# Optimization experiments

Measured on AMD Instinct MI355X. Metric: run time of the kernel, lower is better.

The kernel has to match this reference:

```python
import jax, jax.numpy as jnp
import numpy as np

N = 50000
E = 800000
IN_C = 128
HID = 128
HID2 = 256
OUT_C = 40


def setup_inputs() -> dict:
    key = jax.random.key(0)
    ks = jax.random.split(key, 12)
    x = jax.random.normal(ks[0], (N, IN_C), dtype=jnp.float32)
    edge_index = jax.random.randint(ks[1], (2, E), 0, N, dtype=jnp.int64)
    def lin(k, fi, fo):
        # torch Linear default init: U(-1/sqrt(fi), 1/sqrt(fi))
        b = 1.0 / np.sqrt(fi)
        k1, k2 = jax.random.split(k)
        W = jax.random.uniform(k1, (fi, fo), minval=-b, maxval=b, dtype=jnp.float32)
        bvec = jax.random.uniform(k2, (fo,), minval=-b, maxval=b, dtype=jnp.float32)
        return W, bvec
    W1, b1 = lin(ks[2], IN_C, HID)
    W2, b2 = lin(ks[3], HID, HID)
    W3, b3 = lin(ks[4], HID, HID2)
    W4, b4 = lin(ks[5], HID2, HID2)
    Wl, bl = lin(ks[6], HID2, OUT_C)
    return {"x": x, "edge_index": edge_index,
            "W1": W1, "b1": b1, "W2": W2, "b2": b2,
            "W3": W3, "b3": b3, "W4": W4, "b4": b4,
            "Wl": Wl, "bl": bl}


def gin_conv(x, src, dst, Wa, ba, Wb, bb):
    # GINConv, eps=0: h_i = MLP(x_i + sum_{j->i} x_j)
    agg = jax.ops.segment_sum(x[src], dst, num_segments=N)  # [N, d]
    h = x + agg
    h = jax.nn.relu(h @ Wa + ba)
    return h @ Wb + bb


def reference(x, edge_index, W1, b1, W2, b2, W3, b3, W4, b4, Wl, bl):
    src, dst = edge_index[0], edge_index[1]
    h = jax.nn.relu(gin_conv(x, src, dst, W1, b1, W2, b2))
    # dropout p=0.5 is identity in eval mode
    h = jax.nn.relu(gin_conv(h, src, dst, W3, b3, W4, b4))
    return h @ Wl + bl
```

## Files before the change

### kernel.cpp

```cpp
#include <hip/hip_runtime.h>
#include <hip/hip_bf16.h>
#include <hip/hip_fp16.h>
#include <stdint.h>

#define N_NODES 50000
#define E_EDGES 800000
#define NBKT 196
#define PBUF 6144

typedef short s16x8 __attribute__((ext_vector_type(8)));
typedef _Float16 f16x8 __attribute__((ext_vector_type(8)));
typedef float f32x4 __attribute__((ext_vector_type(4)));

__device__ __forceinline__ unsigned short f2h_bits(float f) {
    return __half_as_ushort(__float2half(f));
}
__device__ __forceinline__ float h2f(unsigned short u) {
    __half h = *reinterpret_cast<const __half*>(&u);
    return __half2float(h);
}
__device__ __forceinline__ float2 h2f2(unsigned int u) {
    __half2 h = *reinterpret_cast<const __half2*>(&u);
    return __half22float2(h);
}

__global__ __launch_bounds__(256) void khist_conv(
    const int* __restrict__ dst, int* __restrict__ gbcnt,
    const float* __restrict__ x, unsigned short* __restrict__ xh) {
    __shared__ int bcnt[NBKT];
    int t = threadIdx.x;
    for (int i = t; i < NBKT; i += 256) bcnt[i] = 0;
    __syncthreads();
    int gid = blockIdx.x * 256 + t;
    const int STRIDE = 256 * 256;
    const float4* xv = (const float4*)x;
    for (int e = gid; e < E_EDGES; e += STRIDE) {
        atomicAdd(&bcnt[dst[e] >> 8], 1);
        float4 a = xv[(size_t)2 * e];
        float4 b = xv[(size_t)2 * e + 1];
        s16x8 h;
        h[0] = (short)f2h_bits(a.x); h[1] = (short)f2h_bits(a.y);
        h[2] = (short)f2h_bits(a.z); h[3] = (short)f2h_bits(a.w);
        h[4] = (short)f2h_bits(b.x); h[5] = (short)f2h_bits(b.y);
        h[6] = (short)f2h_bits(b.z); h[7] = (short)f2h_bits(b.w);
        *(s16x8*)(xh + (size_t)e * 8) = h;
    }
    __syncthreads();
    for (int i = t; i < NBKT; i += 256) atomicAdd(&gbcnt[i], bcnt[i]);
}

__global__ void scan_bkt(const int* __restrict__ gbcnt, int* __restrict__ bscan,
                         int* __restrict__ gcur) {
    __shared__ int wsum[4];
    int t = threadIdx.x, lane = t & 63, wid = t >> 6;
    int v = (t < NBKT) ? gbcnt[t] : 0;
    int x = v;
#pragma unroll
    for (int off = 1; off < 64; off <<= 1) {
        int tt = __shfl_up(x, off);
        if (lane >= off) x += tt;
    }
    if (lane == 63) wsum[wid] = x;
    __syncthreads();
    if (t == 0) {
        int s = 0;
#pragma unroll
        for (int i = 0; i < 4; i++) { int tmp = wsum[i]; wsum[i] = s; s += tmp; }
    }
    __syncthreads();
    int excl = x - v + wsum[wid];
    if (t <= NBKT) bscan[t] = excl;
    if (t < NBKT) gcur[t] = excl;
}

__global__ __launch_bounds__(256) void bin_pass(
    const int* __restrict__ src, const int* __restrict__ dst,
    int* __restrict__ gcur, unsigned int* __restrict__ pool) {
    __shared__ unsigned int lbuf[NBKT][64];
    __shared__ int lcnt[NBKT];
    __shared__ int lbase[NBKT];
    int tid = threadIdx.x;
    for (int i = tid; i < NBKT; i += 256) lcnt[i] = 0;
    __syncthreads();
    const int EPG = (E_EDGES + gridDim.x - 1) / gridDim.x;
    int e0 = blockIdx.x * EPG;
    int e1 = e0 + EPG; if (e1 > E_EDGES) e1 = E_EDGES;
    for (int wbase = e0; wbase < e1; wbase += 2048) {
        int wend = wbase + 2048; if (wend > e1) wend = e1;
        int d8[8], s8[8], n8 = 0;
        {
            int e = wbase + tid;
#pragma unroll
            for (int k = 0; k < 8; k++, e += 256)
                if (e < wend) { d8[n8] = dst[e]; s8[n8] = src[e]; n8++; }
        }
        for (int k = 0; k < n8; k++) {
            int d = d8[k];
            unsigned int rec = (unsigned int)(s8[k] & 0xFFFF) |
                               ((unsigned int)(d & 255) << 16);
            int b = d >> 8;
            int slot = atomicAdd(&lcnt[b], 1);
            if (slot < 64) lbuf[b][slot] = rec;
            else pool[atomicAdd(&gcur[b], 1)] = rec;
        }
        __syncthreads();
        if (tid < NBKT) {
            int c = lcnt[tid]; if (c > 64) c = 64;
            int lines = c >> 5;
            if (lines) lbase[tid] = atomicAdd(&gcur[tid], lines * 32);
        }
        __syncthreads();
        {
            int wid = tid >> 6, lane = tid & 63;
            for (int b = wid * 49; b < (wid + 1) * 49; b++) {
                int c = lcnt[b]; if (c > 64) c = 64;
                int lines = c >> 5, rem = c & 31;
                for (int l = 0; l < lines; l++)
                    if (lane < 32)
                        pool[lbase[b] + l * 32 + lane] = lbuf[b][l * 32 + lane];
                if (lines && lane < rem) lbuf[b][lane] = lbuf[b][lines * 32 + lane];
                if (lane == 0) lcnt[b] = rem;
            }
        }
        __syncthreads();
    }
    if (tid < NBKT) {
        int c = lcnt[tid]; if (c > 64) c = 64;
        if (c) lbase[tid] = atomicAdd(&gcur[tid], c);
    }
    __syncthreads();
    {
        int wid = tid >> 6, lane = tid & 63;
        for (int b = wid * 49; b < (wid + 1) * 49; b++) {
            int c = lcnt[b]; if (c > 64) c = 64;
            if (lane < c) pool[lbase[b] + lane] = lbuf[b][lane];
        }
    }
}

__global__ __launch_bounds__(256) void build_csr(
    const unsigned int* __restrict__ pool, const int* __restrict__ bscan,
    int* __restrict__ rowptr, unsigned short* __restrict__ perm) {
    __shared__ int ncnt[256];
    __shared__ int ncur[256];
    __shared__ int wsum[4];
    __shared__ unsigned short pbuf[PBUF];
    int b = blockIdx.x, t = threadIdx.x;
    int base = bscan[b], K = bscan[b + 1] - base;
    ncnt[t] = 0;
    __syncthreads();
    for (int i = t; i < K; i += 256)
        atomicAdd(&ncnt[(pool[base + i] >> 16) & 255], 1);
    __syncthreads();
    int lane = t & 63, wid = t >> 6;
    int v = ncnt[t], x = v;
#pragma unroll
    for (int off = 1; off < 64; off <<= 1) {
        int tt = __shfl_up(x, off);
        if (lane >= off) x += tt;
    }
    if (lane == 63) wsum[wid] = x;
    __syncthreads();
    if (t == 0) {
        int s = 0;
#pragma unroll
        for (int i = 0; i < 4; i++) { int tmp = wsum[i]; wsum[i] = s; s += tmp; }
    }
    __syncthreads();
    int excl = x - v + wsum[wid];
    int node = b * 256 + t;
    if (node <= N_NODES) rowptr[node] = base + excl;
    ncur[t] = excl;
    __syncthreads();
    for (int i = t; i < K; i += 256) {
        unsigned int rec = pool[base + i];
        int nl = (rec >> 16) & 255;
        int pos = atomicAdd(&ncur[nl], 1);
        if (pos < PBUF) pbuf[pos] = (unsigned short)rec;
        else perm[base + pos] = (unsigned short)rec;
    }
    __syncthreads();
    int KK = K < PBUF ? K : PBUF;
    for (int i = t; i < KK; i += 256) perm[base + i] = pbuf[i];
}

__global__ __launch_bounds__(256) void gather_agg_h(
    const unsigned short* __restrict__ feat,
    const int* __restrict__ rowptr,
    const unsigned short* __restrict__ perm,
    unsigned short* __restrict__ out) {
    int node = (blockIdx.x * 256 + threadIdx.x) >> 6;
    if (node >= N_NODES) return;
    int lane = threadIdx.x & 63;
    const unsigned int* fv = (const unsigned int*)feat;
    float2 acc = h2f2(fv[(size_t)node * 64 + lane]);
    int beg = rowptr[node], end = rowptr[node + 1];
    for (int base = beg; base < end; base += 64) {
        int cnt = end - base; if (cnt > 64) cnt = 64;
        int pv = (base + lane < end) ? (int)perm[base + lane] : 0;
        int j = 0;
        for (; j + 7 < cnt; j += 8) {
            int s0 = __shfl(pv, j);
            int s1 = __shfl(pv, j + 1);
            int s2 = __shfl(pv, j + 2);
            int s3 = __shfl(pv, j + 3);
            int s4 = __shfl(pv, j + 4);
            int s5 = __shfl(pv, j + 5);
            int s6 = __shfl(pv, j + 6);
            int s7 = __shfl(pv, j + 7);
            unsigned int u0 = fv[(size_t)s0 * 64 + lane];
            unsigned int u1 = fv[(size_t)s1 * 64 + lane];
            unsigned int u2 = fv[(size_t)s2 * 64 + lane];
            unsigned int u3 = fv[(size_t)s3 * 64 + lane];
            unsigned int u4 = fv[(size_t)s4 * 64 + lane];
            unsigned int u5 = fv[(size_t)s5 * 64 + lane];
            unsigned int u6 = fv[(size_t)s6 * 64 + lane];
            unsigned int u7 = fv[(size_t)s7 * 64 + lane];
            float2 f0 = h2f2(u0), f1 = h2f2(u1), f2 = h2f2(u2), f3 = h2f2(u3);
            float2 f4 = h2f2(u4), f5 = h2f2(u5), f6 = h2f2(u6), f7 = h2f2(u7);
            acc.x += (f0.x + f1.x) + (f2.x + f3.x);
            acc.y += (f0.y + f1.y) + (f2.y + f3.y);
            acc.x += (f4.x + f5.x) + (f6.x + f7.x);
            acc.y += (f4.y + f5.y) + (f6.y + f7.y);
        }
        for (; j + 1 < cnt; j += 2) {
            int s0 = __shfl(pv, j);
            int s1 = __shfl(pv, j + 1);
            unsigned int u0 = fv[(size_t)s0 * 64 + lane];
            unsigned int u1 = fv[(size_t)s1 * 64 + lane];
            float2 f0 = h2f2(u0), f1 = h2f2(u1);
            acc.x += f0.x + f1.x;
            acc.y += f0.y + f1.y;
        }
        if (j < cnt) {
            int s = __shfl(pv, j);
            float2 f = h2f2(fv[(size_t)s * 64 + lane]);
            acc.x += f.x;
            acc.y += f.y;
        }
    }
    unsigned int o = (unsigned int)f2h_bits(acc.x) | ((unsigned int)f2h_bits(acc.y) << 16);
    ((unsigned int*)out)[(size_t)node * 64 + lane] = o;
}

__device__ __forceinline__ void prep_one(const float* __restrict__ W,
                                         unsigned short* __restrict__ Whi,
                                         unsigned short* __restrict__ Wlo,
                                         int K, int F, int Fpad, int i) {
    int S = K / 32, T = Fpad / 16;
    int total = T * S * 64;
    if (i >= total) return;
    int lane = i & 63;
    int s = (i >> 6) % S;
    int t = (i >> 6) / S;
    int col = t * 16 + (lane & 15);
    int k0 = s * 32 + (lane >> 4) * 8;
    s16x8 vh, vl;
#pragma unroll
    for (int j = 0; j < 8; j++) {
        float w = (col < F) ? W[(size_t)(k0 + j) * F + col] : 0.f;
        unsigned short h = f2h_bits(w);
        float r = (w - h2f(h)) * 1024.0f;
        vh[j] = (short)h;
        vl[j] = (short)f2h_bits(r);
    }
    *(s16x8*)(Whi + (size_t)i * 8) = vh;
    *(s16x8*)(Wlo + (size_t)i * 8) = vl;
}

__global__ void prep_all(const float* W1, const float* W2, const float* W3,
                         const float* W4, const float* Wl,
                         unsigned short* W1h, unsigned short* W1l,
                         unsigned short* W2h, unsigned short* W2l,
                         unsigned short* W3h, unsigned short* W3l,
                         unsigned short* W4h, unsigned short* W4l,
                         unsigned short* Wlh, unsigned short* Wll) {
    int b = blockIdx.x, t = threadIdx.x;
    if (b < 8)       prep_one(W1, W1h, W1l, 128, 128, 128, b * 256 + t);
    else if (b < 16) prep_one(W2, W2h, W2l, 128, 128, 128, (b - 8) * 256 + t);
    else if (b < 32) prep_one(W3, W3h, W3l, 128, 256, 256, (b - 16) * 256 + t);
    else if (b < 64) prep_one(W4, W4h, W4l, 256, 256, 256, (b - 32) * 256 + t);
    else             prep_one(Wl, Wlh, Wll, 256, 40, 64, (b - 64) * 256 + t);
}

template <int K, int F, int FOUT, bool RELU, int RPW, bool HOUT>
__global__ __launch_bounds__(256) void gemm_h(
    const unsigned short* __restrict__ A,
    const unsigned short* __restrict__ Whi,
    const unsigned short* __restrict__ Wlo,
    const float* __restrict__ bias,
    float* __restrict__ out) {
    constexpr int S = K / 32;
    constexpr int T = F / 16;
    constexpr int TL = T / 4;
    int wave = threadIdx.x >> 6;
    int lane = threadIdx.x & 63;
    int row0 = blockIdx.x * (16 * RPW);
    if (row0 >= N_NODES) return;
    int lm = lane & 15;
    int quad = lane >> 4;
    bool rv[RPW];
#pragma unroll
    for (int r = 0; r < RPW; r++) rv[r] = (row0 + r * 16) < N_NODES;

    f16x8 a[RPW][S];
#pragma unroll
    for (int r = 0; r < RPW; r++) {
        int rr = rv[r] ? row0 + r * 16 : row0;
        const unsigned short* ap = A + (size_t)(rr + lm) * K + quad * 8;
#pragma unroll
        for (int s = 0; s < S; s++)
            a[r][s] = *(const f16x8*)(ap + s * 32);
    }

    f32x4 accH[TL][RPW], accL[TL][RPW];
#pragma unroll
    for (int t = 0; t < TL; t++)
#pragma unroll
        for (int r = 0; r < RPW; r++) {
            f32x4 z = {0.f, 0.f, 0.f, 0.f};
            accH[t][r] = z;
            accL[t][r] = z;
        }

#pragma unroll
    for (int s = 0; s < S; s++) {
#pragma unroll
        for (int t = 0; t < TL; t++) {
            int tg = wave * TL + t;
            const size_t fi = (size_t)((tg * S + s) * 64 + lane) * 8;
            const f16x8 bh = *(const f16x8*)(Whi + fi);
            const f16x8 bl = *(const f16x8*)(Wlo + fi);
#pragma unroll
            for (int r = 0; r < RPW; r++) {
                accH[t][r] = __builtin_amdgcn_mfma_f32_16x16x32_f16(a[r][s], bh, accH[t][r], 0, 0, 0);
                accL[t][r] = __builtin_amdgcn_mfma_f32_16x16x32_f16(a[r][s], bl, accL[t][r], 0, 0, 0);
            }
        }
    }

    const float ls = 1.0f / 1024.0f;
#pragma unroll
    for (int r = 0; r < RPW; r++) {
        if (!rv[r]) break;
        int orow = row0 + r * 16 + quad * 4;
#pragma unroll
        for (int t = 0; t < TL; t++) {
            int col = (wave * TL + t) * 16 + lm;
            if (FOUT < F && col >= FOUT) continue;
            float bv = bias[col];
#pragma unroll
            for (int q = 0; q < 4; q++) {
                float vv = fmaf(accL[t][r][q], ls, accH[t][r][q]) + bv;
                if (RELU) vv = fmaxf(vv, 0.f);
                if (HOUT) {
                    ((unsigned short*)out)[(size_t)(orow + q) * FOUT + col] = f2h_bits(vv);
                } else {
                    out[(size_t)(orow + q) * FOUT + col] = vv;
                }
            }
        }
    }
}

extern "C" void kernel_launch(void* const* d_in, const int* in_sizes, int n_in,
                              void* d_out, int out_size, void* d_ws, size_t ws_size,
                              hipStream_t stream) {
    const float* x  = (const float*)d_in[0];
    const int* ei   = (const int*)d_in[1];
    const float* W1 = (const float*)d_in[2];
    const float* b1 = (const float*)d_in[3];
    const float* W2 = (const float*)d_in[4];
    const float* b2 = (const float*)d_in[5];
    const float* W3 = (const float*)d_in[6];
    const float* b3 = (const float*)d_in[7];
    const float* W4 = (const float*)d_in[8];
    const float* b4 = (const float*)d_in[9];
    const float* Wl = (const float*)d_in[10];
    const float* bl = (const float*)d_in[11];
    float* out = (float*)d_out;

    const int* src = ei;
    const int* dst = ei + E_EDGES;

    char* ws = (char*)d_ws;
    size_t off = 0;
    unsigned short* xh  = (unsigned short*)(ws + off); off += (size_t)N_NODES * 128 * 2;
    unsigned short* hFh = (unsigned short*)(ws + off); off += (size_t)N_NODES * 128 * 2;
    unsigned short* h1h = (unsigned short*)(ws + off); off += (size_t)N_NODES * 128 * 2;
    unsigned short* h2h = (unsigned short*)(ws + off); off += (size_t)N_NODES * 256 * 2;
    unsigned short* h2bh= (unsigned short*)(ws + off); off += (size_t)N_NODES * 256 * 2;
    unsigned short* W1h = (unsigned short*)(ws + off); off += 16384 * 2;
    unsigned short* W1l = (unsigned short*)(ws + off); off += 16384 * 2;
    unsigned short* W2h = (unsigned short*)(ws + off); off += 16384 * 2;
    unsigned short* W2l = (unsigned short*)(ws + off); off += 16384 * 2;
    unsigned short* W3h = (unsigned short*)(ws + off); off += 32768 * 2;
    unsigned short* W3l = (unsigned short*)(ws + off); off += 32768 * 2;
    unsigned short* W4h = (unsigned short*)(ws + off); off += 65536 * 2;
    unsigned short* W4l = (unsigned short*)(ws + off); off += 65536 * 2;
    unsigned short* Wlh = (unsigned short*)(ws + off); off += 16384 * 2;
    unsigned short* Wll = (unsigned short*)(ws + off); off += 16384 * 2;
    off = (off + 255) & ~(size_t)255;
    unsigned int* pool = (unsigned int*)(ws + off); off += (size_t)E_EDGES * 4;
    unsigned short* perm = (unsigned short*)(ws + off); off += (size_t)E_EDGES * 2;
    off = (off + 255) & ~(size_t)255;
    int* rowptr = (int*)(ws + off); off += (size_t)(N_NODES + 1) * 4;
    int* gbcnt  = (int*)(ws + off); off += 256 * 4;
    int* bscan  = (int*)(ws + off); off += 256 * 4;
    int* gcur   = (int*)(ws + off); off += 256 * 4;
    (void)ws_size; (void)in_sizes; (void)n_in; (void)out_size;

    (void)hipMemsetAsync(gbcnt, 0, 256 * 4, stream);
    khist_conv<<<256, 256, 0, stream>>>(dst, gbcnt, x, xh);
    scan_bkt<<<1, 256, 0, stream>>>(gbcnt, bscan, gcur);
    bin_pass<<<256, 256, 0, stream>>>(src, dst, gcur, pool);
    build_csr<<<NBKT, 256, 0, stream>>>(pool, bscan, rowptr, perm);

    prep_all<<<72, 256, 0, stream>>>(W1, W2, W3, W4, Wl,
                                     W1h, W1l, W2h, W2l, W3h, W3l,
                                     W4h, W4l, Wlh, Wll);

    const int aggBlocks = (N_NODES * 64 + 255) / 256;
    const int rblk = (N_NODES + 31) / 32;

    gather_agg_h<<<aggBlocks, 256, 0, stream>>>(xh, rowptr, perm, hFh);
    gemm_h<128, 128, 128, true, 2, true><<<rblk, 256, 0, stream>>>(hFh, W1h, W1l, b1, (float*)h1h);
    gemm_h<128, 128, 128, true, 2, true><<<rblk, 256, 0, stream>>>(h1h, W2h, W2l, b2, (float*)xh);

    gather_agg_h<<<aggBlocks, 256, 0, stream>>>(xh, rowptr, perm, hFh);
    gemm_h<128, 256, 256, true, 2, true><<<rblk, 256, 0, stream>>>(hFh, W3h, W3l, b3, (float*)h2h);
    gemm_h<256, 256, 256, true, 2, true><<<rblk, 256, 0, stream>>>(h2h, W4h, W4l, b4, (float*)h2bh);

    gemm_h<256, 64, 40, false, 2, false><<<rblk, 256, 0, stream>>>(h2bh, Wlh, Wll, bl, out);
}
```

Before: 313.4 us.

## Fuse per-layer MLP GEMM chains into single kernels via LDS intermediates

```diff
diff --git a/kernel.cpp b/kernel.cpp
--- a/kernel.cpp
+++ b/kernel.cpp
@@ -283,80 +283,260 @@
     else             prep_one(Wl, Wlh, Wll, 256, 40, 64, (b - 64) * 256 + t);
 }
 
-template <int K, int F, int FOUT, bool RELU, int RPW, bool HOUT>
-__global__ __launch_bounds__(256) void gemm_h(
+
+
+__device__ __forceinline__ void lds_store_h(unsigned short* lds, int C,
+                                            int row, int col, unsigned short v) {
+    int cb = col >> 3, e = col & 7;
+    lds[row * C + (((cb ^ row) & (C / 8 - 1)) << 3) + e] = v;
+}
+__device__ __forceinline__ f16x8 lds_load_frag(const unsigned short* lds, int C,
+                                               int row, int cb) {
+    return *(const f16x8*)(lds + row * C + (((cb ^ row) & (C / 8 - 1)) << 3));
+}
+
+__global__ __launch_bounds__(256) void layer1_mlp(
     const unsigned short* __restrict__ A,
-    const unsigned short* __restrict__ Whi,
-    const unsigned short* __restrict__ Wlo,
-    const float* __restrict__ bias,
+    const unsigned short* __restrict__ W1h, const unsigned short* __restrict__ W1l,
+    const float* __restrict__ b1,
+    const unsigned short* __restrict__ W2h, const unsigned short* __restrict__ W2l,
+    const float* __restrict__ b2,
+    unsigned short* __restrict__ out) {
+    __shared__ unsigned short h1[32 * 128];
+    const int wave = threadIdx.x >> 6, lane = threadIdx.x & 63;
+    const int lm = lane & 15, quad = lane >> 4;
+    const int row0 = blockIdx.x * 32;
+    bool rv1 = (row0 + 16) < N_NODES;
+    const float ls = 1.0f / 1024.0f;
+
+    {
+        f16x8 a[2][4];
+#pragma unroll
+        for (int r = 0; r < 2; r++) {
+            int rr = (r == 0 || rv1) ? row0 + r * 16 : row0;
+            const unsigned short* ap = A + (size_t)(rr + lm) * 128 + quad * 8;
+#pragma unroll
+            for (int s = 0; s < 4; s++) a[r][s] = *(const f16x8*)(ap + s * 32);
+        }
+        f32x4 accH[2][2], accL[2][2];
+#pragma unroll
+        for (int t = 0; t < 2; t++)
+#pragma unroll
+            for (int r = 0; r < 2; r++) {
+                f32x4 z = {0.f, 0.f, 0.f, 0.f};
+                accH[t][r] = z; accL[t][r] = z;
+            }
+#pragma unroll
+        for (int s = 0; s < 4; s++) {
+#pragma unroll
+            for (int t = 0; t < 2; t++) {
+                int tg = wave * 2 + t;
+                const size_t fi = (size_t)((tg * 4 + s) * 64 + lane) * 8;
+                const f16x8 bh = *(const f16x8*)(W1h + fi);
+                const f16x8 bl = *(const f16x8*)(W1l + fi);
+#pragma unroll
+                for (int r = 0; r < 2; r++) {
+                    accH[t][r] = __builtin_amdgcn_mfma_f32_16x16x32_f16(a[r][s], bh, accH[t][r], 0, 0, 0);
+                    accL[t][r] = __builtin_amdgcn_mfma_f32_16x16x32_f16(a[r][s], bl, accL[t][r], 0, 0, 0);
+                }
+            }
+        }
+#pragma unroll
+        for (int r = 0; r < 2; r++)
+#pragma unroll
+            for (int t = 0; t < 2; t++) {
+                int col = (wave * 2 + t) * 16 + lm;
+                float bv = b1[col];
+#pragma unroll
+                for (int q = 0; q < 4; q++) {
+                    float vv = fmaf(accL[t][r][q], ls, accH[t][r][q]) + bv;
+                    vv = fmaxf(vv, 0.f);
+                    lds_store_h(h1, 128, r * 16 + quad * 4 + q, col, f2h_bits(vv));
+                }
+            }
+    }
+    __syncthreads();
+
+    {
+        f32x4 accH[2][2], accL[2][2];
+#pragma unroll
+        for (int t = 0; t < 2; t++)
+#pragma unroll
+            for (int r = 0; r < 2; r++) {
+                f32x4 z = {0.f, 0.f, 0.f, 0.f};
+                accH[t][r] = z; accL[t][r] = z;
+            }
+#pragma unroll
+        for (int s = 0; s < 4; s++) {
+            f16x8 a0 = lds_load_frag(h1, 128, lm, s * 4 + quad);
+            f16x8 a1 = lds_load_frag(h1, 128, 16 + lm, s * 4 + quad);
+#pragma unroll
+            for (int t = 0; t < 2; t++) {
+                int tg = wave * 2 + t;
+                const size_t fi = (size_t)((tg * 4 + s) * 64 + lane) * 8;
+                const f16x8 bh = *(const f16x8*)(W2h + fi);
+                const f16x8 bl = *(const f16x8*)(W2l + fi);
+                accH[t][0] = __builtin_amdgcn_mfma_f32_16x16x32_f16(a0, bh, accH[t][0], 0, 0, 0);
+                accL[t][0] = __builtin_amdgcn_mfma_f32_16x16x32_f16(a0, bl, accL[t][0], 0, 0, 0);
+                accH[t][1] = __builtin_amdgcn_mfma_f32_16x16x32_f16(a1, bh, accH[t][1], 0, 0, 0);
+                accL[t][1] = __builtin_amdgcn_mfma_f32_16x16x32_f16(a1, bl, accL[t][1], 0, 0, 0);
+            }
+        }
+#pragma unroll
+        for (int r = 0; r < 2; r++) {
+            if (r == 1 && !rv1) break;
+            int orow = row0 + r * 16 + quad * 4;
+#pragma unroll
+            for (int t = 0; t < 2; t++) {
+                int col = (wave * 2 + t) * 16 + lm;
+                float bv = b2[col];
+#pragma unroll
+                for (int q = 0; q < 4; q++) {
+                    float vv = fmaf(accL[t][r][q], ls, accH[t][r][q]) + bv;
+                    vv = fmaxf(vv, 0.f);
+                    out[(size_t)(orow + q) * 128 + col] = f2h_bits(vv);
+                }
+            }
+        }
+    }
+}
+
+__global__ __launch_bounds__(256) void layer2_mlp(
+    const unsigned short* __restrict__ A,
+    const unsigned short* __restrict__ W3h, const unsigned short* __restrict__ W3l,
+    const float* __restrict__ b3,
+    const unsigned short* __restrict__ W4h, const unsigned short* __restrict__ W4l,
+    const float* __restrict__ b4,
+    const unsigned short* __restrict__ Wlh, const unsigned short* __restrict__ Wll,
+    const float* __restrict__ bl,
     float* __restrict__ out) {
-    constexpr int S = K / 32;
-    constexpr int T = F / 16;
-    constexpr int TL = T / 4;
-    int wave = threadIdx.x >> 6;
-    int lane = threadIdx.x & 63;
-    int row0 = blockIdx.x * (16 * RPW);
-    if (row0 >= N_NODES) return;
-    int lm = lane & 15;
-    int quad = lane >> 4;
-    bool rv[RPW];
-#pragma unroll
-    for (int r = 0; r < RPW; r++) rv[r] = (row0 + r * 16) < N_NODES;
-
-    f16x8 a[RPW][S];
-#pragma unroll
-    for (int r = 0; r < RPW; r++) {
-        int rr = rv[r] ? row0 + r * 16 : row0;
-        const unsigned short* ap = A + (size_t)(rr + lm) * K + quad * 8;
-#pragma unroll
-        for (int s = 0; s < S; s++)
-            a[r][s] = *(const f16x8*)(ap + s * 32);
-    }
-
-    f32x4 accH[TL][RPW], accL[TL][RPW];
-#pragma unroll
-    for (int t = 0; t < TL; t++)
-#pragma unroll
-        for (int r = 0; r < RPW; r++) {
+    __shared__ unsigned short h2[32 * 256];
+    __shared__ unsigned short h2b[32 * 256];
+    const int wave = threadIdx.x >> 6, lane = threadIdx.x & 63;
+    const int lm = lane & 15, quad = lane >> 4;
+    const int row0 = blockIdx.x * 32;
+    bool rv1 = (row0 + 16) < N_NODES;
+    const float ls = 1.0f / 1024.0f;
+
+    {
+        f16x8 a[2][4];
+#pragma unroll
+        for (int r = 0; r < 2; r++) {
+            int rr = (r == 0 || rv1) ? row0 + r * 16 : row0;
+            const unsigned short* ap = A + (size_t)(rr + lm) * 128 + quad * 8;
+#pragma unroll
+            for (int s = 0; s < 4; s++) a[r][s] = *(const f16x8*)(ap + s * 32);
+        }
+        f32x4 accH[4][2], accL[4][2];
+#pragma unroll
+        for (int t = 0; t < 4; t++)
+#pragma unroll
+            for (int r = 0; r < 2; r++) {
+                f32x4 z = {0.f, 0.f, 0.f, 0.f};
+                accH[t][r] = z; accL[t][r] = z;
+            }
+#pragma unroll
+        for (int s = 0; s < 4; s++) {
+#pragma unroll
+            for (int t = 0; t < 4; t++) {
+                int tg = wave * 4 + t;
+                const size_t fi = (size_t)((tg * 4 + s) * 64 + lane) * 8;
+                const f16x8 bh = *(const f16x8*)(W3h + fi);
+                const f16x8 bl = *(const f16x8*)(W3l + fi);
+#pragma unroll
+                for (int r = 0; r < 2; r++) {
+                    accH[t][r] = __builtin_amdgcn_mfma_f32_16x16x32_f16(a[r][s], bh, accH[t][r], 0, 0, 0);
+                    accL[t][r] = __builtin_amdgcn_mfma_f32_16x16x32_f16(a[r][s], bl, accL[t][r], 0, 0, 0);
+                }
+            }
+        }
+#pragma unroll
+        for (int r = 0; r < 2; r++)
+#pragma unroll
+            for (int t = 0; t < 4; t++) {
+                int col = (wave * 4 + t) * 16 + lm;
+                float bv = b3[col];
+#pragma unroll
+                for (int q = 0; q < 4; q++) {
+                    float vv = fmaf(accL[t][r][q], ls, accH[t][r][q]) + bv;
+                    vv = fmaxf(vv, 0.f);
+                    lds_store_h(h2, 256, r * 16 + quad * 4 + q, col, f2h_bits(vv));
+                }
+            }
+    }
+    __syncthreads();
+
+    {
+        f32x4 accH[4][2], accL[4][2];
+#pragma unroll
+        for (int t = 0; t < 4; t++)
+#pragma unroll
+            for (int r = 0; r < 2; r++) {
+                f32x4 z = {0.f, 0.f, 0.f, 0.f};
+                accH[t][r] = z; accL[t][r] = z;
+            }
+#pragma unroll
+        for (int s = 0; s < 8; s++) {
+            f16x8 a0 = lds_load_frag(h2, 256, lm, s * 4 + quad);
+            f16x8 a1 = lds_load_frag(h2, 256, 16 + lm, s * 4 + quad);
+#pragma unroll
+            for (int t = 0; t < 4; t++) {
+                int tg = wave * 4 + t;
+                const size_t fi = (size_t)((tg * 8 + s) * 64 + lane) * 8;
+                const f16x8 bh = *(const f16x8*)(W4h + fi);
+                const f16x8 bl = *(const f16x8*)(W4l + fi);
+                accH[t][0] = __builtin_amdgcn_mfma_f32_16x16x32_f16(a0, bh, accH[t][0], 0, 0, 0);
+                accL[t][0] = __builtin_amdgcn_mfma_f32_16x16x32_f16(a0, bl, accL[t][0], 0, 0, 0);
+                accH[t][1] = __builtin_amdgcn_mfma_f32_16x16x32_f16(a1, bh, accH[t][1], 0, 0, 0);
+                accL[t][1] = __builtin_amdgcn_mfma_f32_16x16x32_f16(a1, bl, accL[t][1], 0, 0, 0);
+            }
+        }
+        __syncthreads();
+#pragma unroll
+        for (int r = 0; r < 2; r++)
+#pragma unroll
+            for (int t = 0; t < 4; t++) {
+                int col = (wave * 4 + t) * 16 + lm;
+                float bv = b4[col];
+#pragma unroll
+                for (int q = 0; q < 4; q++) {
+                    float vv = fmaf(accL[t][r][q], ls, accH[t][r][q]) + bv;
+                    vv = fmaxf(vv, 0.f);
+                    lds_store_h(h2b, 256, r * 16 + quad * 4 + q, col, f2h_bits(vv));
+                }
+            }
+    }
+    __syncthreads();
+
+    {
+        f32x4 accH[2], accL[2];
+        {
             f32x4 z = {0.f, 0.f, 0.f, 0.f};
-            accH[t][r] = z;
-            accL[t][r] = z;
-        }
-
-#pragma unroll
-    for (int s = 0; s < S; s++) {
-#pragma unroll
-        for (int t = 0; t < TL; t++) {
-            int tg = wave * TL + t;
-            const size_t fi = (size_t)((tg * S + s) * 64 + lane) * 8;
-            const f16x8 bh = *(const f16x8*)(Whi + fi);
-            const f16x8 bl = *(const f16x8*)(Wlo + fi);
-#pragma unroll
-            for (int r = 0; r < RPW; r++) {
-                accH[t][r] = __builtin_amdgcn_mfma_f32_16x16x32_f16(a[r][s], bh, accH[t][r], 0, 0, 0);
-                accL[t][r] = __builtin_amdgcn_mfma_f32_16x16x32_f16(a[r][s], bl, accL[t][r], 0, 0, 0);
-            }
-        }
-    }
-
-    const float ls = 1.0f / 1024.0f;
-#pragma unroll
-    for (int r = 0; r < RPW; r++) {
-        if (!rv[r]) break;
-        int orow = row0 + r * 16 + quad * 4;
-#pragma unroll
-        for (int t = 0; t < TL; t++) {
-            int col = (wave * TL + t) * 16 + lm;
-            if (FOUT < F && col >= FOUT) continue;
-            float bv = bias[col];
-#pragma unroll
-            for (int q = 0; q < 4; q++) {
-                float vv = fmaf(accL[t][r][q], ls, accH[t][r][q]) + bv;
-                if (RELU) vv = fmaxf(vv, 0.f);
-                if (HOUT) {
-                    ((unsigned short*)out)[(size_t)(orow + q) * FOUT + col] = f2h_bits(vv);
-                } else {
-                    out[(size_t)(orow + q) * FOUT + col] = vv;
+            accH[0] = z; accH[1] = z; accL[0] = z; accL[1] = z;
+        }
+#pragma unroll
+        for (int s = 0; s < 8; s++) {
+            f16x8 a0 = lds_load_frag(h2b, 256, lm, s * 4 + quad);
+            f16x8 a1 = lds_load_frag(h2b, 256, 16 + lm, s * 4 + quad);
+            const size_t fi = (size_t)((wave * 8 + s) * 64 + lane) * 8;
+            const f16x8 bh = *(const f16x8*)(Wlh + fi);
+            const f16x8 bl = *(const f16x8*)(Wll + fi);
+            accH[0] = __builtin_amdgcn_mfma_f32_16x16x32_f16(a0, bh, accH[0], 0, 0, 0);
+            accL[0] = __builtin_amdgcn_mfma_f32_16x16x32_f16(a0, bl, accL[0], 0, 0, 0);
+            accH[1] = __builtin_amdgcn_mfma_f32_16x16x32_f16(a1, bh, accH[1], 0, 0, 0);
+            accL[1] = __builtin_amdgcn_mfma_f32_16x16x32_f16(a1, bl, accL[1], 0, 0, 0);
+        }
+        int col = wave * 16 + lm;
+        if (col < 40) {
+            float bv = bl[col];
+#pragma unroll
+            for (int r = 0; r < 2; r++) {
+                if (r == 1 && !rv1) break;
+                int orow = row0 + r * 16 + quad * 4;
+#pragma unroll
+                for (int q = 0; q < 4; q++) {
+                    float vv = fmaf(accL[r][q], ls, accH[r][q]) + bv;
+                    out[(size_t)(orow + q) * 40 + col] = vv;
                 }
             }
         }
@@ -387,9 +567,6 @@
     size_t off = 0;
     unsigned short* xh  = (unsigned short*)(ws + off); off += (size_t)N_NODES * 128 * 2;
     unsigned short* hFh = (unsigned short*)(ws + off); off += (size_t)N_NODES * 128 * 2;
-    unsigned short* h1h = (unsigned short*)(ws + off); off += (size_t)N_NODES * 128 * 2;
-    unsigned short* h2h = (unsigned short*)(ws + off); off += (size_t)N_NODES * 256 * 2;
-    unsigned short* h2bh= (unsigned short*)(ws + off); off += (size_t)N_NODES * 256 * 2;
     unsigned short* W1h = (unsigned short*)(ws + off); off += 16384 * 2;
     unsigned short* W1l = (unsigned short*)(ws + off); off += 16384 * 2;
     unsigned short* W2h = (unsigned short*)(ws + off); off += 16384 * 2;
@@ -424,12 +601,9 @@
     const int rblk = (N_NODES + 31) / 32;
 
     gather_agg_h<<<aggBlocks, 256, 0, stream>>>(xh, rowptr, perm, hFh);
-    gemm_h<128, 128, 128, true, 2, true><<<rblk, 256, 0, stream>>>(hFh, W1h, W1l, b1, (float*)h1h);
-    gemm_h<128, 128, 128, true, 2, true><<<rblk, 256, 0, stream>>>(h1h, W2h, W2l, b2, (float*)xh);
+    layer1_mlp<<<rblk, 256, 0, stream>>>(hFh, W1h, W1l, b1, W2h, W2l, b2, xh);
 
     gather_agg_h<<<aggBlocks, 256, 0, stream>>>(xh, rowptr, perm, hFh);
-    gemm_h<128, 256, 256, true, 2, true><<<rblk, 256, 0, stream>>>(hFh, W3h, W3l, b3, (float*)h2h);
-    gemm_h<256, 256, 256, true, 2, true><<<rblk, 256, 0, stream>>>(h2h, W4h, W4l, b4, (float*)h2bh);
-
-    gemm_h<256, 64, 40, false, 2, false><<<rblk, 256, 0, stream>>>(h2bh, Wlh, Wll, bl, out);
-}
+    layer2_mlp<<<rblk, 256, 0, stream>>>(hFh, W3h, W3l, b3, W4h, W4l, b4,
+                                         Wlh, Wll, bl, out);
+}
```

Result: faster. 277.9 us (-11.3%).
